# Kernel optimization log

Measured on AMD Instinct MI355X. Metric: run time of the kernel, lower is better.

## Reference

```python
import jax, jax.numpy as jnp
import numpy as np

B, N, F_IN = 8, 1024, 256
N_HEADS, N_HIDDEN = 8, 32  # out_features=256, is_concat=True -> n_hidden = 256//8
NEG_SLOPE = 0.2


def setup_inputs() -> dict:
    key = jax.random.key(0)
    k1, k2, k3 = jax.random.split(key, 3)
    vertex = jax.random.normal(k1, (B, N, F_IN), dtype=jnp.float32)
    # linear_vert.weight.T  (applied as x @ w_vert)
    w_vert = jax.random.normal(k2, (F_IN, N_HEADS * N_HIDDEN), dtype=jnp.float32) / np.sqrt(F_IN)
    # attn linear: [2*n_hidden] -> 1, no bias; shared across heads
    attn_w = jax.random.normal(k3, (2 * N_HIDDEN,), dtype=jnp.float32) / np.sqrt(2 * N_HIDDEN)
    return {"vertex": vertex, "w_vert": w_vert, "attn_w": attn_w}


def reference(vertex, w_vert, attn_w):
    b, n, _ = vertex.shape
    # g_vertex: [b, n, h, d]
    g = jnp.einsum("bni,io->bno", vertex, w_vert).reshape(b, n, N_HEADS, N_HIDDEN)
    # attn(cat([g_i, g_j])) == g_i . w_src + g_j . w_dst  (cat index i = repeat_interleave half)
    w_src, w_dst = attn_w[:N_HIDDEN], attn_w[N_HIDDEN:]
    s_src = jnp.einsum("bnhd,d->bnh", g, w_src)  # [b, n, h]
    s_dst = jnp.einsum("bnhd,d->bnh", g, w_dst)  # [b, n, h]
    # e[b,i,j,h] = LeakyReLU(s_src[b,i,h] + s_dst[b,j,h])
    e = s_src[:, :, None, :] + s_dst[:, None, :, :]
    e = jnp.where(e >= 0, e, NEG_SLOPE * e)
    # softmax over j (dim=-2 after squeeze in the torch code)
    a = jax.nn.softmax(e, axis=2)  # [b, i, j, h]
    # dropout in eval mode = identity
    out = jnp.einsum("bijh,bjhd->bihd", a, g)  # [b, n, h, d]
    return out.reshape(b, n, N_HEADS * N_HIDDEN)
```

## Files before the change

### kernel.cpp

```cpp
#include <hip/hip_runtime.h>
#include <hip/hip_bf16.h>
#include <hip/hip_fp16.h>
#include <math.h>


#define F_IN  256
#define NOUT  256
#define NB    8
#define NN    1024
#define NH    8
#define ND    32
#define NROWS (NB * NN)
#define LOG2E 1.44269504f

typedef __attribute__((ext_vector_type(8))) short bf16x8;
typedef __attribute__((ext_vector_type(8))) _Float16 f16x8;
typedef __attribute__((ext_vector_type(2))) _Float16 f16x2;
typedef __attribute__((ext_vector_type(4))) float f32x4;

__device__ inline unsigned pk_bf16(float a, float b) {
    union { __hip_bfloat162 h2; unsigned u; } c;
    c.h2 = __float22bfloat162_rn(make_float2(a, b));
    return c.u;
}
__device__ inline unsigned pk_f16(float a, float b) {
    union { __half2 h2; unsigned u; } c;
    c.h2 = __float22half2_rn(make_float2(a, b));
    return c.u;
}
__device__ inline void split8(const float4 va, const float4 vb,
                              bf16x8& hi, bf16x8& lo) {
    float f[8] = {va.x, va.y, va.z, va.w, vb.x, vb.y, vb.z, vb.w};
    union { bf16x8 v; unsigned u[4]; } H, L;
    #pragma unroll
    for (int i = 0; i < 4; ++i) {
        unsigned u0 = __float_as_uint(f[2 * i]);
        unsigned u1 = __float_as_uint(f[2 * i + 1]);
        unsigned h0 = u0 & 0xFFFF0000u;
        unsigned h1 = u1 & 0xFFFF0000u;
        H.u[i] = (u0 >> 16) | h1;
        L.u[i] = pk_bf16(f[2 * i]     - __uint_as_float(h0),
                         f[2 * i + 1] - __uint_as_float(h1));
    }
    hi = H.v; lo = L.v;
}

__global__ __launch_bounds__(256, 4) void gat_gemm_kernel(
    const float* __restrict__ vertex, const float* __restrict__ w_vert,
    const float* __restrict__ attn_w, unsigned short* __restrict__ gT,
    float* __restrict__ ssT, float* __restrict__ sdT)
{
    __shared__ __align__(16) unsigned short bHi[8192];
    __shared__ __align__(16) unsigned short bLo[8192];
    f32x4 (*comb)[4][64] = reinterpret_cast<f32x4(*)[4][64]>(bHi);
    unsigned short (*trans)[72] = reinterpret_cast<unsigned short(*)[72]>(bLo);

    const int t = threadIdx.x, lane = t & 63, wv = t >> 6;
    const int mt = wv & 1, kh = wv >> 1;
    const int il = lane & 15, ql = lane >> 4;
    const int h = blockIdx.y, gr0 = blockIdx.x * 64;
    const int b = gr0 >> 10, bh = b * NH + h;

    {
        const int n  = t & 31;
        const int kb = t >> 5;
        const int il_s = n & 15, nt_s = n >> 4;
        #pragma unroll
        for (int q = 0; q < 4; ++q) {
            const int k0 = kb * 8 + 64 * q;
            const float* wp = w_vert + (size_t)k0 * NOUT + h * 32 + n;
            float f[8];
            #pragma unroll
            for (int j = 0; j < 8; ++j) f[j] = wp[j * NOUT];
            unsigned hu[4], lu[4];
            #pragma unroll
            for (int j2 = 0; j2 < 4; ++j2) {
                unsigned u0 = __float_as_uint(f[2 * j2]);
                unsigned u1 = __float_as_uint(f[2 * j2 + 1]);
                unsigned h0 = u0 & 0xFFFF0000u;
                unsigned h1 = u1 & 0xFFFF0000u;
                hu[j2] = (u0 >> 16) | h1;
                lu[j2] = pk_bf16(f[2 * j2]     - __uint_as_float(h0),
                                 f[2 * j2 + 1] - __uint_as_float(h1));
            }
            const int ktile = k0 >> 5;
            const int qlb   = (k0 & 31) >> 3;
            const int off   = (ktile * 2 + nt_s) * 512 + (qlb * 16 + il_s) * 8;
            *(uint4*)&bHi[off] = *(const uint4*)hu;
            *(uint4*)&bLo[off] = *(const uint4*)lu;
        }
    }
    __syncthreads();

    const float* arow0 = vertex + (size_t)(gr0 + mt * 32 + il) * F_IN + kh * 128 + ql * 8;
    const float* arow1 = arow0 + 16 * F_IN;

    f32x4 c00 = {0.f, 0.f, 0.f, 0.f}, c01 = c00, c10 = c00, c11 = c00;

    #pragma unroll
    for (int kk = 0; kk < 4; ++kk) {
        float4 a0a = *(const float4*)(arow0 + kk * 32);
        float4 a0b = *(const float4*)(arow0 + kk * 32 + 4);
        float4 a1a = *(const float4*)(arow1 + kk * 32);
        float4 a1b = *(const float4*)(arow1 + kk * 32 + 4);

        const int bkb = (kh * 4 + kk) * 2;
        bf16x8 bh0 = *(const bf16x8*)&bHi[bkb * 512 + lane * 8];
        bf16x8 bh1 = *(const bf16x8*)&bHi[(bkb + 1) * 512 + lane * 8];
        bf16x8 bl0 = *(const bf16x8*)&bLo[bkb * 512 + lane * 8];
        bf16x8 bl1 = *(const bf16x8*)&bLo[(bkb + 1) * 512 + lane * 8];

        bf16x8 a0hi, a0lo, a1hi, a1lo;
        split8(a0a, a0b, a0hi, a0lo);
        split8(a1a, a1b, a1hi, a1lo);

        c00 = __builtin_amdgcn_mfma_f32_16x16x32_bf16(a0hi, bh0, c00, 0, 0, 0);
        c01 = __builtin_amdgcn_mfma_f32_16x16x32_bf16(a0hi, bh1, c01, 0, 0, 0);
        c10 = __builtin_amdgcn_mfma_f32_16x16x32_bf16(a1hi, bh0, c10, 0, 0, 0);
        c11 = __builtin_amdgcn_mfma_f32_16x16x32_bf16(a1hi, bh1, c11, 0, 0, 0);
        c00 = __builtin_amdgcn_mfma_f32_16x16x32_bf16(a0lo, bh0, c00, 0, 0, 0);
        c01 = __builtin_amdgcn_mfma_f32_16x16x32_bf16(a0lo, bh1, c01, 0, 0, 0);
        c10 = __builtin_amdgcn_mfma_f32_16x16x32_bf16(a1lo, bh0, c10, 0, 0, 0);
        c11 = __builtin_amdgcn_mfma_f32_16x16x32_bf16(a1lo, bh1, c11, 0, 0, 0);
        c00 = __builtin_amdgcn_mfma_f32_16x16x32_bf16(a0hi, bl0, c00, 0, 0, 0);
        c01 = __builtin_amdgcn_mfma_f32_16x16x32_bf16(a0hi, bl1, c01, 0, 0, 0);
        c10 = __builtin_amdgcn_mfma_f32_16x16x32_bf16(a1hi, bl0, c10, 0, 0, 0);
        c11 = __builtin_amdgcn_mfma_f32_16x16x32_bf16(a1hi, bl1, c11, 0, 0, 0);
    }

    __syncthreads();
    if (kh == 1) {
        comb[mt][0][lane] = c00; comb[mt][1][lane] = c01;
        comb[mt][2][lane] = c10; comb[mt][3][lane] = c11;
    }
    __syncthreads();
    if (kh == 0) {
        c00 = c00 + comb[mt][0][lane]; c01 = c01 + comb[mt][1][lane];
        c10 = c10 + comb[mt][2][lane]; c11 = c11 + comb[mt][3][lane];

        const float wsv0 = attn_w[il],      wsv1 = attn_w[16 + il];
        const float wdv0 = attn_w[ND + il], wdv1 = attn_w[ND + 16 + il];
        const int j0 = (gr0 & 1023) + mt * 32;

        #pragma unroll
        for (int g = 0; g < 2; ++g) {
            f32x4 cA = g ? c10 : c00;
            f32x4 cB = g ? c11 : c01;
            const int jl = mt * 32 + g * 16 + ql * 4;

            *(unsigned*)&trans[il][jl]          = pk_f16(cA[0], cA[1]);
            *(unsigned*)&trans[il][jl + 2]      = pk_f16(cA[2], cA[3]);
            *(unsigned*)&trans[16 + il][jl]     = pk_f16(cB[0], cB[1]);
            *(unsigned*)&trans[16 + il][jl + 2] = pk_f16(cB[2], cB[3]);

            const int jr = j0 + g * 16 + ql * 4;
            #pragma unroll
            for (int reg = 0; reg < 4; ++reg) {
                float ps = cA[reg] * wsv0 + cB[reg] * wsv1;
                float pd = cA[reg] * wdv0 + cB[reg] * wdv1;
                #pragma unroll
                for (int off = 1; off < 16; off <<= 1) {
                    ps += __shfl_xor(ps, off);
                    pd += __shfl_xor(pd, off);
                }
                if (il == 0) {
                    ssT[bh * NN + jr + reg] = ps;
                    sdT[bh * NN + jr + reg] = pd;
                }
            }
        }
    }
    __syncthreads();

    {
        const int d  = t >> 3;
        const int jo = (t & 7) * 8;
        uint4 v = *(const uint4*)&trans[d][jo];
        *(uint4*)(gT + ((size_t)(bh * ND) + d) * NN + (gr0 & 1023) + jo) = v;
    }
}

__global__ __launch_bounds__(256, 4) void gat_attn_kernel(
    const unsigned short* __restrict__ gT, const float* __restrict__ ssT,
    const float* __restrict__ sdT, float* __restrict__ out)
{
    __shared__ __align__(16) unsigned short BpH[NN];
    __shared__ __align__(16) unsigned short BnH[NN];
    __shared__ f32x4 ccomb[2][12][64];
    __shared__ float red[4];

    const int bid = blockIdx.x;
    const int bh = bid & 63;
    const int b = bh >> 3, h = bh & 7;
    const int i0 = (bid >> 6) * 64;
    const int t = threadIdx.x, lane = t & 63, jq = t >> 6;
    const int il = lane & 15, ql = lane >> 4;

    float sdv[4]; float M = -3.0e38f;
    #pragma unroll
    for (int q = 0; q < 4; ++q) {
        sdv[q] = sdT[bh * NN + t + 256 * q];
        M = fmaxf(M, sdv[q]);
    }
    #pragma unroll
    for (int off = 32; off >= 1; off >>= 1)
        M = fmaxf(M, __shfl_xor(M, off));
    if (lane == 0) red[jq] = M;
    #pragma unroll
    for (int q = 0; q < 4; ++q) {
        union { _Float16 h; unsigned short u; } cp, cn;
        cp.h = (_Float16)exp2f(sdv[q] * LOG2E);
        cn.h = (_Float16)exp2f(0.2f * LOG2E * sdv[q]);
        BpH[t + 256 * q] = cp.u;
        BnH[t + 256 * q] = cn.u;
    }
    __syncthreads();
    M = fmaxf(fmaxf(red[0], red[1]), fmaxf(red[2], red[3]));

    f16x2 apv[4], anv[4];
    #pragma unroll
    for (int mt = 0; mt < 4; ++mt) {
        const float si = ssT[bh * NN + i0 + mt * 16 + il];
        float x = si + M; x = fmaxf(x, 0.2f * x);
        const float mk = x * LOG2E;
        const _Float16 ah = (_Float16)exp2f(fmaf(si, LOG2E, -mk));
        const _Float16 nh = (_Float16)exp2f(fmaf(0.2f * si, LOG2E, -mk));
        apv[mt] = (f16x2){ah, ah};
        anv[mt] = (f16x2){nh, nh};
    }

    const unsigned short* gb0 = gT + ((size_t)(bh * ND) + il) * NN + jq * 256 + ql * 8;
    const unsigned short* gb1 = gb0 + 16 * NN;
    const unsigned short* bpq = BpH + jq * 256 + ql * 8;
    const unsigned short* bnq = BnH + jq * 256 + ql * 8;

    union { f16x8 v; unsigned u[4]; } ones;
    ones.u[0] = ones.u[1] = ones.u[2] = ones.u[3] = 0x3C003C00u;

    f32x4 c0[4], c1[4], cs[4];
    #pragma unroll
    for (int mt = 0; mt < 4; ++mt) {
        c0[mt] = (f32x4){0.f, 0.f, 0.f, 0.f};
        c1[mt] = c0[mt]; cs[mt] = c0[mt];
    }

    #pragma unroll 2
    for (int kk = 0; kk < 256; kk += 32) {
        union { uint4 q; unsigned w[4]; } pw, nw;
        pw.q = *(const uint4*)(bpq + kk);
        nw.q = *(const uint4*)(bnq + kk);
        const f16x8 bf0 = *(const f16x8*)(gb0 + kk);
        const f16x8 bf1 = *(const f16x8*)(gb1 + kk);

        #pragma unroll
        for (int mt = 0; mt < 4; ++mt) {
            union { f16x8 v; unsigned u[4]; } af;
            #pragma unroll
            for (int u = 0; u < 4; ++u) {
                union { unsigned w; f16x2 v; } p2, n2, e2;
                p2.w = pw.w[u];
                n2.w = nw.w[u];
                e2.v = __builtin_elementwise_max(p2.v * apv[mt],
                                                 n2.v * anv[mt]);
                af.u[u] = e2.w;
            }
            c0[mt] = __builtin_amdgcn_mfma_f32_16x16x32_f16(af.v, bf0, c0[mt], 0, 0, 0);
            c1[mt] = __builtin_amdgcn_mfma_f32_16x16x32_f16(af.v, bf1, c1[mt], 0, 0, 0);
            cs[mt] = __builtin_amdgcn_mfma_f32_16x16x32_f16(af.v, ones.v, cs[mt], 0, 0, 0);
        }
    }

    if (jq >= 2) {
        #pragma unroll
        for (int mt = 0; mt < 4; ++mt) {
            ccomb[jq - 2][mt * 3 + 0][lane] = c0[mt];
            ccomb[jq - 2][mt * 3 + 1][lane] = c1[mt];
            ccomb[jq - 2][mt * 3 + 2][lane] = cs[mt];
        }
    }
    __syncthreads();
    if (jq < 2) {
        #pragma unroll
        for (int mt = 0; mt < 4; ++mt) {
            c0[mt] = c0[mt] + ccomb[jq][mt * 3 + 0][lane];
            c1[mt] = c1[mt] + ccomb[jq][mt * 3 + 1][lane];
            cs[mt] = cs[mt] + ccomb[jq][mt * 3 + 2][lane];
        }
    }
    __syncthreads();
    if (jq == 1) {
        #pragma unroll
        for (int mt = 0; mt < 4; ++mt) {
            ccomb[0][mt * 3 + 0][lane] = c0[mt];
            ccomb[0][mt * 3 + 1][lane] = c1[mt];
            ccomb[0][mt * 3 + 2][lane] = cs[mt];
        }
    }
    __syncthreads();
    if (jq == 0) {
        #pragma unroll
        for (int mt = 0; mt < 4; ++mt) {
            c0[mt] = c0[mt] + ccomb[0][mt * 3 + 0][lane];
            c1[mt] = c1[mt] + ccomb[0][mt * 3 + 1][lane];
            cs[mt] = cs[mt] + ccomb[0][mt * 3 + 2][lane];

            float* ob = out + (size_t)(b * NN + i0 + mt * 16 + ql * 4) * NOUT + h * ND + il;
            #pragma unroll
            for (int reg = 0; reg < 4; ++reg) {
                const float r = 1.0f / cs[mt][reg];
                ob[reg * NOUT]      = c0[mt][reg] * r;
                ob[reg * NOUT + 16] = c1[mt][reg] * r;
            }
        }
    }
}

extern "C" void kernel_launch(void* const* d_in, const int* in_sizes, int n_in,
                              void* d_out, int out_size, void* d_ws, size_t ws_size,
                              hipStream_t stream) {
    (void)in_sizes; (void)n_in; (void)out_size; (void)ws_size;
    const float* vertex = (const float*)d_in[0];
    const float* w_vert = (const float*)d_in[1];
    const float* attn_w = (const float*)d_in[2];
    float* out = (float*)d_out;

    char* ws = (char*)d_ws;
    unsigned short* gT = (unsigned short*)ws;
    float* ssT = (float*)(ws + ((size_t)NB * NH * ND * NN * 2));
    float* sdT = ssT + (size_t)NB * NH * NN;

    gat_gemm_kernel<<<dim3(128, NH), 256, 0, stream>>>(vertex, w_vert, attn_w,
                                                       gT, ssT, sdT);
    gat_attn_kernel<<<1024, 256, 0, stream>>>(gT, ssT, sdT, out);
}
```

Before: 85.21 us.

## Precompute exp tables in GEMM kernel, halve attention row tile, drop ones-MFMA

The projection kernel now computes the per-node exp2 tables (positive and negative slope) in fp16 and writes them to workspace, so each attention block no longer recomputes 2048 exponentials. The attention kernel tiles 32 query rows instead of 64 with double the grid and higher launch-bound occupancy. The row-sum MFMA against a ones vector is replaced by fdot2 accumulation plus shuffles. The max is now derived from fp16 exp values via log2, which loses some precision and may risk overflow edge cases. Smaller tiles mean each block rereads gT for fewer rows.

```diff
diff --git a/kernel.cpp b/kernel.cpp
--- a/kernel.cpp
+++ b/kernel.cpp
@@ -28,6 +28,27 @@
     c.h2 = __float22half2_rn(make_float2(a, b));
     return c.u;
 }
+__device__ inline unsigned short f16b(float x) {
+    union { __half h; unsigned short u; } c;
+    c.h = __float2half(x);
+    return c.u;
+}
+__device__ inline float h2f(unsigned short u) {
+    union { unsigned short u; __half h; } c;
+    c.u = u;
+    return __half2float(c.h);
+}
+
+#if __has_builtin(__builtin_amdgcn_fdot2)
+__device__ __forceinline__ float fdot2acc(f16x2 a, f16x2 b, float c) {
+    return __builtin_amdgcn_fdot2(a, b, c, false);
+}
+#else
+__device__ __forceinline__ float fdot2acc(f16x2 a, f16x2 b, float c) {
+    return c + (float)a.x * (float)b.x + (float)a.y * (float)b.y;
+}
+#endif
+
 __device__ inline void split8(const float4 va, const float4 vb,
                               bf16x8& hi, bf16x8& lo) {
     float f[8] = {va.x, va.y, va.z, va.w, vb.x, vb.y, vb.z, vb.w};
@@ -48,7 +69,8 @@
 __global__ __launch_bounds__(256, 4) void gat_gemm_kernel(
     const float* __restrict__ vertex, const float* __restrict__ w_vert,
     const float* __restrict__ attn_w, unsigned short* __restrict__ gT,
-    float* __restrict__ ssT, float* __restrict__ sdT)
+    float* __restrict__ ssT, unsigned short* __restrict__ BpH,
+    unsigned short* __restrict__ BnH)
 {
     __shared__ __align__(16) unsigned short bHi[8192];
     __shared__ __align__(16) unsigned short bLo[8192];
@@ -154,6 +176,8 @@
             *(unsigned*)&trans[16 + il][jl + 2] = pk_f16(cB[2], cB[3]);
 
             const int jr = j0 + g * 16 + ql * 4;
+            float psv[4];
+            unsigned short bpv[4], bnv[4];
             #pragma unroll
             for (int reg = 0; reg < 4; ++reg) {
                 float ps = cA[reg] * wsv0 + cB[reg] * wsv1;
@@ -163,10 +187,17 @@
                     ps += __shfl_xor(ps, off);
                     pd += __shfl_xor(pd, off);
                 }
-                if (il == 0) {
-                    ssT[bh * NN + jr + reg] = ps;
-                    sdT[bh * NN + jr + reg] = pd;
-                }
+                psv[reg] = ps;
+                bpv[reg] = f16b(exp2f(pd * LOG2E));
+                bnv[reg] = f16b(exp2f(0.2f * LOG2E * pd));
+            }
+            if (il == 0) {
+                *(float4*)(ssT + bh * NN + jr) =
+                    make_float4(psv[0], psv[1], psv[2], psv[3]);
+                *(ushort4*)(BpH + bh * NN + jr) =
+                    make_ushort4(bpv[0], bpv[1], bpv[2], bpv[3]);
+                *(ushort4*)(BnH + bh * NN + jr) =
+                    make_ushort4(bnv[0], bnv[1], bnv[2], bnv[3]);
             }
         }
     }
@@ -180,49 +211,43 @@
     }
 }
 
-__global__ __launch_bounds__(256, 4) void gat_attn_kernel(
+__global__ __launch_bounds__(256, 8) void gat_attn_kernel(
     const unsigned short* __restrict__ gT, const float* __restrict__ ssT,
-    const float* __restrict__ sdT, float* __restrict__ out)
+    const unsigned short* __restrict__ BpH,
+    const unsigned short* __restrict__ BnH, float* __restrict__ out)
 {
-    __shared__ __align__(16) unsigned short BpH[NN];
-    __shared__ __align__(16) unsigned short BnH[NN];
-    __shared__ f32x4 ccomb[2][12][64];
+    __shared__ f32x4 ccomb[2][4][64];
+    __shared__ float scomb[2][2][64];
     __shared__ float red[4];
 
     const int bid = blockIdx.x;
     const int bh = bid & 63;
     const int b = bh >> 3, h = bh & 7;
-    const int i0 = (bid >> 6) * 64;
+    const int i0 = (bid >> 6) * 32;
     const int t = threadIdx.x, lane = t & 63, jq = t >> 6;
     const int il = lane & 15, ql = lane >> 4;
 
-    float sdv[4]; float M = -3.0e38f;
-    #pragma unroll
-    for (int q = 0; q < 4; ++q) {
-        sdv[q] = sdT[bh * NN + t + 256 * q];
-        M = fmaxf(M, sdv[q]);
+    const unsigned short* bpb = BpH + (size_t)bh * NN;
+    const unsigned short* bnb = BnH + (size_t)bh * NN;
+
+    float bm;
+    {
+        ushort4 v = *(const ushort4*)(bpb + t * 4);
+        bm = fmaxf(fmaxf(h2f(v.x), h2f(v.y)), fmaxf(h2f(v.z), h2f(v.w)));
     }
     #pragma unroll
     for (int off = 32; off >= 1; off >>= 1)
-        M = fmaxf(M, __shfl_xor(M, off));
-    if (lane == 0) red[jq] = M;
-    #pragma unroll
-    for (int q = 0; q < 4; ++q) {
-        union { _Float16 h; unsigned short u; } cp, cn;
-        cp.h = (_Float16)exp2f(sdv[q] * LOG2E);
-        cn.h = (_Float16)exp2f(0.2f * LOG2E * sdv[q]);
-        BpH[t + 256 * q] = cp.u;
-        BnH[t + 256 * q] = cn.u;
-    }
-    __syncthreads();
-    M = fmaxf(fmaxf(red[0], red[1]), fmaxf(red[2], red[3]));
-
-    f16x2 apv[4], anv[4];
-    #pragma unroll
-    for (int mt = 0; mt < 4; ++mt) {
+        bm = fmaxf(bm, __shfl_xor(bm, off));
+    if (lane == 0) red[jq] = bm;
+    __syncthreads();
+    bm = fmaxf(fmaxf(red[0], red[1]), fmaxf(red[2], red[3]));
+    const float Mlog2 = log2f(bm);
+    f16x2 apv[2], anv[2];
+    #pragma unroll
+    for (int mt = 0; mt < 2; ++mt) {
         const float si = ssT[bh * NN + i0 + mt * 16 + il];
-        float x = si + M; x = fmaxf(x, 0.2f * x);
-        const float mk = x * LOG2E;
+        const float t2 = fmaf(si, LOG2E, Mlog2);
+        const float mk = fmaxf(t2, 0.2f * t2);
         const _Float16 ah = (_Float16)exp2f(fmaf(si, LOG2E, -mk));
         const _Float16 nh = (_Float16)exp2f(fmaf(0.2f * si, LOG2E, -mk));
         apv[mt] = (f16x2){ah, ah};
@@ -231,17 +256,17 @@
 
     const unsigned short* gb0 = gT + ((size_t)(bh * ND) + il) * NN + jq * 256 + ql * 8;
     const unsigned short* gb1 = gb0 + 16 * NN;
-    const unsigned short* bpq = BpH + jq * 256 + ql * 8;
-    const unsigned short* bnq = BnH + jq * 256 + ql * 8;
-
-    union { f16x8 v; unsigned u[4]; } ones;
-    ones.u[0] = ones.u[1] = ones.u[2] = ones.u[3] = 0x3C003C00u;
-
-    f32x4 c0[4], c1[4], cs[4];
-    #pragma unroll
-    for (int mt = 0; mt < 4; ++mt) {
+    const unsigned short* bpq = bpb + jq * 256 + ql * 8;
+    const unsigned short* bnq = bnb + jq * 256 + ql * 8;
+
+    const f16x2 one2 = (f16x2){(_Float16)1.0f, (_Float16)1.0f};
+
+    f32x4 c0[2], c1[2];
+    float S[2] = {0.f, 0.f};
+    #pragma unroll
+    for (int mt = 0; mt < 2; ++mt) {
         c0[mt] = (f32x4){0.f, 0.f, 0.f, 0.f};
-        c1[mt] = c0[mt]; cs[mt] = c0[mt];
+        c1[mt] = c0[mt];
     }
 
     #pragma unroll 2
@@ -253,8 +278,9 @@
         const f16x8 bf1 = *(const f16x8*)(gb1 + kk);
 
         #pragma unroll
-        for (int mt = 0; mt < 4; ++mt) {
+        for (int mt = 0; mt < 2; ++mt) {
             union { f16x8 v; unsigned u[4]; } af;
+            float s = S[mt];
             #pragma unroll
             for (int u = 0; u < 4; ++u) {
                 union { unsigned w; f16x2 v; } p2, n2, e2;
@@ -263,51 +289,56 @@
                 e2.v = __builtin_elementwise_max(p2.v * apv[mt],
                                                  n2.v * anv[mt]);
                 af.u[u] = e2.w;
-            }
+                s = fdot2acc(e2.v, one2, s);
+            }
+            S[mt] = s;
             c0[mt] = __builtin_amdgcn_mfma_f32_16x16x32_f16(af.v, bf0, c0[mt], 0, 0, 0);
             c1[mt] = __builtin_amdgcn_mfma_f32_16x16x32_f16(af.v, bf1, c1[mt], 0, 0, 0);
-            cs[mt] = __builtin_amdgcn_mfma_f32_16x16x32_f16(af.v, ones.v, cs[mt], 0, 0, 0);
         }
     }
 
     if (jq >= 2) {
         #pragma unroll
-        for (int mt = 0; mt < 4; ++mt) {
-            ccomb[jq - 2][mt * 3 + 0][lane] = c0[mt];
-            ccomb[jq - 2][mt * 3 + 1][lane] = c1[mt];
-            ccomb[jq - 2][mt * 3 + 2][lane] = cs[mt];
+        for (int mt = 0; mt < 2; ++mt) {
+            ccomb[jq - 2][mt * 2 + 0][lane] = c0[mt];
+            ccomb[jq - 2][mt * 2 + 1][lane] = c1[mt];
+            scomb[jq - 2][mt][lane] = S[mt];
         }
     }
     __syncthreads();
     if (jq < 2) {
         #pragma unroll
-        for (int mt = 0; mt < 4; ++mt) {
-            c0[mt] = c0[mt] + ccomb[jq][mt * 3 + 0][lane];
-            c1[mt] = c1[mt] + ccomb[jq][mt * 3 + 1][lane];
-            cs[mt] = cs[mt] + ccomb[jq][mt * 3 + 2][lane];
+        for (int mt = 0; mt < 2; ++mt) {
+            c0[mt] = c0[mt] + ccomb[jq][mt * 2 + 0][lane];
+            c1[mt] = c1[mt] + ccomb[jq][mt * 2 + 1][lane];
+            S[mt] += scomb[jq][mt][lane];
         }
     }
     __syncthreads();
     if (jq == 1) {
         #pragma unroll
-        for (int mt = 0; mt < 4; ++mt) {
-            ccomb[0][mt * 3 + 0][lane] = c0[mt];
-            ccomb[0][mt * 3 + 1][lane] = c1[mt];
-            ccomb[0][mt * 3 + 2][lane] = cs[mt];
+        for (int mt = 0; mt < 2; ++mt) {
+            ccomb[0][mt * 2 + 0][lane] = c0[mt];
+            ccomb[0][mt * 2 + 1][lane] = c1[mt];
+            scomb[0][mt][lane] = S[mt];
         }
     }
     __syncthreads();
     if (jq == 0) {
         #pragma unroll
-        for (int mt = 0; mt < 4; ++mt) {
-            c0[mt] = c0[mt] + ccomb[0][mt * 3 + 0][lane];
-            c1[mt] = c1[mt] + ccomb[0][mt * 3 + 1][lane];
-            cs[mt] = cs[mt] + ccomb[0][mt * 3 + 2][lane];
+        for (int mt = 0; mt < 2; ++mt) {
+            c0[mt] = c0[mt] + ccomb[0][mt * 2 + 0][lane];
+            c1[mt] = c1[mt] + ccomb[0][mt * 2 + 1][lane];
+            S[mt] += scomb[0][mt][lane];
+            S[mt] += __shfl_xor(S[mt], 16);
+            S[mt] += __shfl_xor(S[mt], 32);
 
             float* ob = out + (size_t)(b * NN + i0 + mt * 16 + ql * 4) * NOUT + h * ND + il;
             #pragma unroll
             for (int reg = 0; reg < 4; ++reg) {
-                const float r = 1.0f / cs[mt][reg];
+                const int rr = ql * 4 + reg;
+                const float Srow = __shfl(S[mt], (ql << 4) | rr);
+                const float r = 1.0f / Srow;
                 ob[reg * NOUT]      = c0[mt][reg] * r;
                 ob[reg * NOUT + 16] = c1[mt][reg] * r;
             }
@@ -326,10 +357,14 @@
 
     char* ws = (char*)d_ws;
     unsigned short* gT = (unsigned short*)ws;
-    float* ssT = (float*)(ws + ((size_t)NB * NH * ND * NN * 2));
-    float* sdT = ssT + (size_t)NB * NH * NN;
+    char* p = ws + (size_t)NB * NH * ND * NN * 2;
+    float* ssT = (float*)p;
+    p += (size_t)NB * NH * NN * 4;
+    unsigned short* BpH = (unsigned short*)p;
+    p += (size_t)NB * NH * NN * 2;
+    unsigned short* BnH = (unsigned short*)p;
 
     gat_gemm_kernel<<<dim3(128, NH), 256, 0, stream>>>(vertex, w_vert, attn_w,
-                                                       gT, ssT, sdT);
-    gat_attn_kernel<<<1024, 256, 0, stream>>>(gT, ssT, sdT, out);
-}
+                                                       gT, ssT, BpH, BnH);
+    gat_attn_kernel<<<2048, 256, 0, stream>>>(gT, ssT, BpH, BnH, out);
+}
```

New measurement: 96.51 us. 13.3% more time.
